# Optimization experiments

Measured on AMD Instinct MI355X. Metric: run time of the kernel, lower is better.

Reference implementation:

```python
import jax, jax.numpy as jnp
import numpy as np

D = 2048; Nl = 2; Nh = 32; Nkv = 8; V = 32000; Dh = 5632; Lm = 4096
B = 1; L = 2048; E = 1e-5
DHEAD = D // Nh  # 64


def setup_inputs() -> dict:
    key = jax.random.key(0)
    ks = jax.random.split(key, 10)
    s = 0.02
    rn = lambda k, shape: jax.random.normal(k, shape, jnp.float32) * s
    emb = rn(ks[0], (V, D))
    wq = rn(ks[1], (Nl, D, D))
    wk = rn(ks[2], (Nl, D, D * Nkv // Nh))
    wv = rn(ks[3], (Nl, D, D * Nkv // Nh))
    wa = rn(ks[4], (Nl, D, D))
    wg = rn(ks[5], (Nl, D, Dh))
    wu = rn(ks[6], (Nl, D, Dh))
    wd = rn(ks[7], (Nl, Dh, D))
    w_an = jnp.ones((Nl, D), jnp.float32)
    w_fn = jnp.ones((Nl, D), jnp.float32)
    w_on = jnp.ones((D,), jnp.float32)
    w_out = rn(ks[8], (D, V))
    # RoPE tables (interleaved-pair convention, matching reshape(..., -1, 2))
    theta = 1.0 / (10000.0 ** (jnp.arange(0, DHEAD, 2, dtype=jnp.float32) / DHEAD))
    freqs = jnp.outer(jnp.arange(Lm, dtype=jnp.float32), theta)  # [Lm, DHEAD//2]
    cos = jnp.cos(freqs)
    sin = jnp.sin(freqs)
    ti = jax.random.randint(ks[9], (B, L), 0, V)
    return dict(ti=ti, emb=emb, wq=wq, wk=wk, wv=wv, wa=wa, w_an=w_an, w_fn=w_fn,
                wg=wg, wu=wu, wd=wd, w_on=w_on, w_out=w_out, cos=cos, sin=sin)


def _rmsnorm(x, w):
    return x * jax.lax.rsqrt(jnp.mean(x * x, -1, keepdims=True) + E) * w


def _rope(x, cos, sin):
    # x: [B, L, H, DHEAD]; cos/sin: [1, L, 1, DHEAD//2]; interleaved pairs
    xs = x.reshape(*x.shape[:-1], DHEAD // 2, 2)
    xr, xi = xs[..., 0], xs[..., 1]
    r1 = xr * cos - xi * sin
    i1 = xr * sin + xi * cos
    return jnp.stack([r1, i1], axis=-1).reshape(x.shape)


def reference(ti, emb, wq, wk, wv, wa, w_an, w_fn, wg, wu, wd, w_on, w_out, cos, sin):
    cos_l = cos[:L].reshape(1, L, 1, DHEAD // 2)
    sin_l = sin[:L].reshape(1, L, 1, DHEAD // 2)
    mask = jnp.triu(jnp.full((1, 1, L, L), -jnp.inf, jnp.float32), 1)
    scale = 1.0 / jnp.sqrt(jnp.float32(DHEAD))
    rep = Nh // Nkv
    x = emb[ti]  # [B, L, D]
    for l in range(Nl):
        h = _rmsnorm(x, w_an[l])
        q = (h @ wq[l]).reshape(B, L, Nh, DHEAD)
        k = (h @ wk[l]).reshape(B, L, Nkv, DHEAD)
        v = (h @ wv[l]).reshape(B, L, Nkv, DHEAD)
        q = _rope(q, cos_l, sin_l)
        k = _rope(k, cos_l, sin_l)
        kx = jnp.repeat(k, rep, axis=2)  # GQA expand -> [B, L, Nh, DHEAD]
        vx = jnp.repeat(v, rep, axis=2)
        a = jnp.einsum('blhd,bmhd->bhlm', q, kx) * scale
        p = jax.nn.softmax(a + mask, axis=-1)
        sa = jnp.einsum('bhlm,bmhd->blhd', p, vx).reshape(B, L, D)
        x = x + sa @ wa[l]
        hf = _rmsnorm(x, w_fn[l])
        x = x + (jax.nn.silu(hf @ wg[l]) * (hf @ wu[l])) @ wd[l]
    return _rmsnorm(x, w_on) @ w_out  # [B, L, V]
```

## Files before the change

kernel.cpp:

```cpp
#include <hip/hip_runtime.h>
#include <hip/hip_bf16.h>

#define DMODEL 2048
#define LSEQ   2048
#define NHEAD  32
#define NKVH   8
#define DHEAD  64
#define DFF    5632
#define VOCAB  32000

typedef __attribute__((ext_vector_type(8))) short bf16x8;
typedef __attribute__((ext_vector_type(4))) float f32x4;
typedef __attribute__((ext_vector_type(8))) unsigned short ushort8;

__device__ __forceinline__ void gload_lds16(const __hip_bfloat16* g, __hip_bfloat16* l) {
  __builtin_amdgcn_global_load_lds((const void __attribute__((address_space(1)))*)g,
                                   (void __attribute__((address_space(3)))*)l, 16, 0, 0);
}

__device__ __forceinline__ float bfbits2f(unsigned short u) {
  return __uint_as_float(((unsigned int)u) << 16);
}
__device__ __forceinline__ unsigned short f2bfbits(float f) {
  unsigned int x = __float_as_uint(f);
  return (unsigned short)((x + 0x7fffu + ((x >> 16) & 1u)) >> 16);
}

__global__ __launch_bounds__(256) void embed_k(const int* __restrict__ ti,
                                               const float* __restrict__ emb,
                                               float* __restrict__ x) {
  const int row = blockIdx.x;
  const int t = threadIdx.x;
  const int tok = ti[row];
  const float4* s = (const float4*)(emb + (size_t)tok * DMODEL);
  float4* d = (float4*)(x + (size_t)row * DMODEL);
  d[t] = s[t];
  d[t + 256] = s[t + 256];
}

__global__ __launch_bounds__(256) void rmsnorm_k(const float* __restrict__ x,
                                                 const float* __restrict__ w,
                                                 __hip_bfloat16* __restrict__ out) {
  const int row = blockIdx.x;
  const int t = threadIdx.x;
  const float4* xr = (const float4*)(x + (size_t)row * DMODEL);
  float4 a = xr[t];
  float4 b = xr[t + 256];
  float ss = a.x*a.x + a.y*a.y + a.z*a.z + a.w*a.w
           + b.x*b.x + b.y*b.y + b.z*b.z + b.w*b.w;
  #pragma unroll
  for (int m = 32; m >= 1; m >>= 1) ss += __shfl_xor(ss, m);
  __shared__ float red[4];
  if ((t & 63) == 0) red[t >> 6] = ss;
  __syncthreads();
  const float tot = red[0] + red[1] + red[2] + red[3];
  const float sc = rsqrtf(tot * (1.0f / DMODEL) + 1e-5f);
  const float4* w4 = (const float4*)w;
  float4 wa_ = w4[t], wb_ = w4[t + 256];
  __hip_bfloat16* o = out + (size_t)row * DMODEL;
  o[4*t + 0] = __float2bfloat16(a.x * sc * wa_.x);
  o[4*t + 1] = __float2bfloat16(a.y * sc * wa_.y);
  o[4*t + 2] = __float2bfloat16(a.z * sc * wa_.z);
  o[4*t + 3] = __float2bfloat16(a.w * sc * wa_.w);
  o[1024 + 4*t + 0] = __float2bfloat16(b.x * sc * wb_.x);
  o[1024 + 4*t + 1] = __float2bfloat16(b.y * sc * wb_.y);
  o[1024 + 4*t + 2] = __float2bfloat16(b.z * sc * wb_.z);
  o[1024 + 4*t + 3] = __float2bfloat16(b.w * sc * wb_.w);
}

__global__ __launch_bounds__(256) void transpose_k(const float* __restrict__ src,
                                                   __hip_bfloat16* __restrict__ dst,
                                                   int K, int N) {
  __shared__ float tile[64 * 65];
  const int kb = blockIdx.x * 64;
  const int nb = blockIdx.y * 64;
  const int t = threadIdx.x;
  #pragma unroll
  for (int i = 0; i < 16; ++i) {
    const int idx = t + 256 * i;
    const int r = idx >> 6, c = idx & 63;
    tile[r * 65 + c] = src[(size_t)(kb + r) * N + nb + c];
  }
  __syncthreads();
  #pragma unroll
  for (int i = 0; i < 16; ++i) {
    const int idx = t + 256 * i;
    const int n = idx >> 6, k = idx & 63;
    dst[(size_t)(nb + n) * K + kb + k] = __float2bfloat16(tile[k * 65 + n]);
  }
}

template <int EPI>
__global__ __launch_bounds__(256) void gemm_bt(const __hip_bfloat16* __restrict__ A,
                                               const __hip_bfloat16* __restrict__ Bt,
                                               float* __restrict__ Cf,
                                               __hip_bfloat16* __restrict__ Cb,
                                               int M, int N, int K) {
  __shared__ __align__(16) __hip_bfloat16 As[128 * 32];
  __shared__ __align__(16) __hip_bfloat16 Bs[128 * 32];
  const int tid = threadIdx.x;
  const int wave = tid >> 6;
  const int lane = tid & 63;
  const int nbx = M >> 7;
  const int nwg = nbx * (N >> 7);
  const int orig = blockIdx.y * nbx + blockIdx.x;
  const int wid = (orig & 7) * (nwg >> 3) + (orig >> 3);
  const int tm = (wid % nbx) << 7;
  const int tn = (wid / nbx) << 7;
  const int wr = (wave >> 1) * 64;
  const int wc = (wave & 1) * 64;
  const int fr = lane & 15;
  const int fg = lane >> 4;
  const f32x4 fzero = {0.f, 0.f, 0.f, 0.f};
  f32x4 acc[4][4];
  #pragma unroll
  for (int i = 0; i < 4; ++i)
    #pragma unroll
    for (int j = 0; j < 4; ++j) acc[i][j] = fzero;
  const int srow = wave * 32 + (lane >> 2);
  const int scol = (lane & 3) * 8;
  const __hip_bfloat16* gA = A + (size_t)(tm + srow) * K + scol;
  const __hip_bfloat16* gB = Bt + (size_t)(tn + srow) * K + scol;
  __hip_bfloat16* lA = &As[wave * 1024];
  __hip_bfloat16* lB = &Bs[wave * 1024];
  for (int k0 = 0; k0 < K; k0 += 32) {
    gload_lds16(gA, lA);
    gload_lds16(gA + (size_t)16 * K, lA + 512);
    gload_lds16(gB, lB);
    gload_lds16(gB + (size_t)16 * K, lB + 512);
    gA += 32; gB += 32;
    __syncthreads();
    bf16x8 af[4], bfr[4];
    #pragma unroll
    for (int i = 0; i < 4; ++i) af[i] = *(const bf16x8*)&As[(wr + i * 16 + fr) * 32 + fg * 8];
    #pragma unroll
    for (int j = 0; j < 4; ++j) bfr[j] = *(const bf16x8*)&Bs[(wc + j * 16 + fr) * 32 + fg * 8];
    #pragma unroll
    for (int i = 0; i < 4; ++i)
      #pragma unroll
      for (int j = 0; j < 4; ++j)
        acc[i][j] = __builtin_amdgcn_mfma_f32_16x16x32_bf16(af[i], bfr[j], acc[i][j], 0, 0, 0);
    __syncthreads();
  }
  #pragma unroll
  for (int i = 0; i < 4; ++i)
    #pragma unroll
    for (int j = 0; j < 4; ++j)
      #pragma unroll
      for (int r = 0; r < 4; ++r) {
        const int row = tm + wr + i * 16 + fg * 4 + r;
        const int col = tn + wc + j * 16 + fr;
        const float v = acc[i][j][r];
        if (EPI == 0) Cf[(size_t)row * N + col] = v;
        else if (EPI == 1) Cb[(size_t)row * N + col] = __float2bfloat16(v);
        else Cf[(size_t)row * N + col] += v;
      }
}

template <int EPI>
__global__ __launch_bounds__(512, 2) void gemm8p(const __hip_bfloat16* __restrict__ A,
                                                 const __hip_bfloat16* __restrict__ Bt,
                                                 float* __restrict__ Cf,
                                                 __hip_bfloat16* __restrict__ Cb,
                                                 int M, int N, int K) {
  __shared__ __align__(16) __hip_bfloat16 lds[2][2][256 * 64];
  const int tid = threadIdx.x;
  const int wave = tid >> 6;
  const int lane = tid & 63;
  const int nbx = M >> 8;
  const int nwg = nbx * (N >> 8);
  const int orig = blockIdx.y * nbx + blockIdx.x;
  const int wid = (orig & 7) * (nwg >> 3) + (orig >> 3);
  const int tm = (wid % nbx) << 8;
  const int tn = (wid / nbx) << 8;
  const int wm = wave >> 2;
  const int wn = wave & 3;
  const int fr = lane & 15;
  const int fg = lane >> 4;
  const int l3 = lane >> 3;
  const int l7 = lane & 7;
  const int swzcol = (l3 ^ l7) << 3;
  const size_t sK = (size_t)K;

  const __hip_bfloat16* pA = A + (size_t)(tm + wave * 8 + l3) * sK + swzcol;
  const __hip_bfloat16* pB = Bt + (size_t)(tn + wave * 8 + l3) * sK + swzcol;

  #pragma unroll
  for (int j = 0; j < 4; ++j) {
    gload_lds16(pA + (size_t)(j * 64) * sK, &lds[0][0][(j * 64 + wave * 8) * 64]);
    gload_lds16(pB + (size_t)(j * 64) * sK, &lds[0][1][(j * 64 + wave * 8) * 64]);
  }
  pA += 64; pB += 64;
  #pragma unroll
  for (int j = 0; j < 4; ++j) {
    gload_lds16(pA + (size_t)(j * 64) * sK, &lds[1][0][(j * 64 + wave * 8) * 64]);
    gload_lds16(pB + (size_t)(j * 64) * sK, &lds[1][1][(j * 64 + wave * 8) * 64]);
  }
  pA += 64; pB += 64;

  const f32x4 fzero = {0.f, 0.f, 0.f, 0.f};
  f32x4 acc[8][4];
  #pragma unroll
  for (int i = 0; i < 8; ++i)
    #pragma unroll
    for (int j = 0; j < 4; ++j) acc[i][j] = fzero;

  const int wmo = wm * 128;
  const int wno = wn * 64;
  const int rswz = (fr & 7) << 4;
  const int ct0 = ((fg * 16) ^ rswz) >> 1;
  const int ct1 = ((64 + fg * 16) ^ rswz) >> 1;

  asm volatile("s_waitcnt vmcnt(8)" ::: "memory");
  __builtin_amdgcn_s_barrier();
  __builtin_amdgcn_sched_barrier(0);

  const int NT = K >> 6;
  for (int kt = 0; kt < NT; ++kt) {
    const int cur = kt & 1;
    const __hip_bfloat16* LA = &lds[cur][0][0];
    const __hip_bfloat16* LB = &lds[cur][1][0];
    bf16x8 av[8][2], bv[4][2];
    #pragma unroll
    for (int mi = 0; mi < 8; ++mi) {
      av[mi][0] = *(const bf16x8*)&LA[(wmo + mi * 16 + fr) * 64 + ct0];
      av[mi][1] = *(const bf16x8*)&LA[(wmo + mi * 16 + fr) * 64 + ct1];
    }
    #pragma unroll
    for (int ni = 0; ni < 4; ++ni) {
      bv[ni][0] = *(const bf16x8*)&LB[(wno + ni * 16 + fr) * 64 + ct0];
      bv[ni][1] = *(const bf16x8*)&LB[(wno + ni * 16 + fr) * 64 + ct1];
    }
    asm volatile("s_waitcnt lgkmcnt(0)" ::: "memory");
    __builtin_amdgcn_sched_barrier(0);
    __builtin_amdgcn_s_barrier();
    __builtin_amdgcn_sched_barrier(0);
    const bool pre = (kt + 2 < NT);
    #pragma unroll
    for (int q = 0; q < 4; ++q) {
      if (pre) {
        gload_lds16(pA + (size_t)(q * 64) * sK, &lds[cur][0][(q * 64 + wave * 8) * 64]);
        gload_lds16(pB + (size_t)(q * 64) * sK, &lds[cur][1][(q * 64 + wave * 8) * 64]);
      }
      const int mb = (q & 1) * 4;
      const int nb = (q >> 1) * 2;
      __builtin_amdgcn_s_setprio(1);
      #pragma unroll
      for (int mi = 0; mi < 4; ++mi)
        #pragma unroll
        for (int ni = 0; ni < 2; ++ni) {
          acc[mb + mi][nb + ni] = __builtin_amdgcn_mfma_f32_16x16x32_bf16(
              av[mb + mi][0], bv[nb + ni][0], acc[mb + mi][nb + ni], 0, 0, 0);
          acc[mb + mi][nb + ni] = __builtin_amdgcn_mfma_f32_16x16x32_bf16(
              av[mb + mi][1], bv[nb + ni][1], acc[mb + mi][nb + ni], 0, 0, 0);
        }
      __builtin_amdgcn_s_setprio(0);
    }
    if (pre) { pA += 64; pB += 64; }
    if (kt + 1 < NT) {
      if (pre) asm volatile("s_waitcnt vmcnt(8)" ::: "memory");
      else     asm volatile("s_waitcnt vmcnt(0)" ::: "memory");
      __builtin_amdgcn_s_barrier();
      __builtin_amdgcn_sched_barrier(0);
    }
  }
  #pragma unroll
  for (int mf = 0; mf < 8; ++mf)
    #pragma unroll
    for (int nf = 0; nf < 4; ++nf)
      #pragma unroll
      for (int r = 0; r < 4; ++r) {
        const int row = tm + wmo + mf * 16 + fg * 4 + r;
        const int col = tn + wno + nf * 16 + fr;
        const float v = acc[mf][nf][r];
        if (EPI == 0) Cf[(size_t)row * N + col] = v;
        else if (EPI == 1) Cb[(size_t)row * N + col] = __float2bfloat16(v);
        else Cf[(size_t)row * N + col] += v;
      }
}

__global__ __launch_bounds__(256) void rope_k(__hip_bfloat16* __restrict__ qkv,
                                              const float* __restrict__ cosT,
                                              const float* __restrict__ sinT) {
  const int row = blockIdx.x;
  const int t = threadIdx.x;
  unsigned int* base = (unsigned int*)(qkv + (size_t)row * 3072);
  #pragma unroll
  for (int p = t; p < 1280; p += 256) {
    const int hp = p >> 5;
    const int i = p & 31;
    const unsigned int packed = base[hp * 32 + i];
    const float x0 = bfbits2f((unsigned short)(packed & 0xffffu));
    const float x1 = bfbits2f((unsigned short)(packed >> 16));
    const float c = cosT[row * 32 + i];
    const float s = sinT[row * 32 + i];
    const float r0 = x0 * c - x1 * s;
    const float r1 = x0 * s + x1 * c;
    base[hp * 32 + i] = (unsigned int)f2bfbits(r0) | ((unsigned int)f2bfbits(r1) << 16);
  }
}

__global__ __launch_bounds__(256) void attn_k(const __hip_bfloat16* __restrict__ qkv,
                                              __hip_bfloat16* __restrict__ out) {
  const int h = blockIdx.x;
  const int qt = blockIdx.y;
  const int tid = threadIdx.x;
  const int wave = tid >> 6;
  const int lane = tid & 63;
  const int fr = lane & 15;
  const int fg = lane >> 4;
  const int qb = qt * 64;
  const int kcol = DMODEL + (h >> 2) * DHEAD;
  const int vcol = DMODEL + NKVH * DHEAD + (h >> 2) * DHEAD;
  __shared__ __align__(16) __hip_bfloat16 Ks[64 * 72];
  __shared__ __align__(16) __hip_bfloat16 Vt[64 * 72];
  __shared__ __align__(16) __hip_bfloat16 Ps[4][16 * 72];
  bf16x8 qf[2];
  {
    const __hip_bfloat16* qp = qkv + (size_t)(qb + wave * 16 + fr) * 3072 + h * DHEAD + fg * 8;
    qf[0] = *(const bf16x8*)qp;
    qf[1] = *(const bf16x8*)(qp + 32);
  }
  const f32x4 fzero = {0.f, 0.f, 0.f, 0.f};
  float m_run[4], l_run[4];
  f32x4 o[4];
  #pragma unroll
  for (int r = 0; r < 4; ++r) { m_run[r] = -1e30f; l_run[r] = 0.f; }
  #pragma unroll
  for (int c = 0; c < 4; ++c) o[c] = fzero;

  const int sr = tid >> 2;
  const int sc = (tid & 3) * 16;
  for (int t = 0; t <= qt; ++t) {
    const __hip_bfloat16* kp = qkv + (size_t)(t * 64 + sr) * 3072 + kcol + sc;
    *(float4*)&Ks[sr * 72 + sc] = *(const float4*)kp;
    *(float4*)&Ks[sr * 72 + sc + 8] = *(const float4*)(kp + 8);
    const __hip_bfloat16* vp = qkv + (size_t)(t * 64 + sr) * 3072 + vcol + sc;
    ushort8 v0 = *(const ushort8*)vp;
    ushort8 v1 = *(const ushort8*)(vp + 8);
    unsigned short* vt = (unsigned short*)Vt;
    #pragma unroll
    for (int i = 0; i < 8; ++i) {
      vt[(sc + i) * 72 + sr] = v0[i];
      vt[(sc + 8 + i) * 72 + sr] = v1[i];
    }
    __syncthreads();
    f32x4 s[4];
    #pragma unroll
    for (int c = 0; c < 4; ++c) {
      s[c] = fzero;
      #pragma unroll
      for (int ks = 0; ks < 2; ++ks) {
        bf16x8 kf = *(const bf16x8*)&Ks[(c * 16 + fr) * 72 + ks * 32 + fg * 8];
        s[c] = __builtin_amdgcn_mfma_f32_16x16x32_bf16(qf[ks], kf, s[c], 0, 0, 0);
      }
    }
    const int rowg = qb + wave * 16 + fg * 4;
    #pragma unroll
    for (int c = 0; c < 4; ++c)
      #pragma unroll
      for (int r = 0; r < 4; ++r) {
        float v = s[c][r] * 0.125f;
        if (t * 64 + c * 16 + fr > rowg + r) v = -1e30f;
        s[c][r] = v;
      }
    #pragma unroll
    for (int r = 0; r < 4; ++r) {
      float pm = fmaxf(fmaxf(s[0][r], s[1][r]), fmaxf(s[2][r], s[3][r]));
      pm = fmaxf(pm, __shfl_xor(pm, 1));
      pm = fmaxf(pm, __shfl_xor(pm, 2));
      pm = fmaxf(pm, __shfl_xor(pm, 4));
      pm = fmaxf(pm, __shfl_xor(pm, 8));
      const float mn = fmaxf(m_run[r], pm);
      const float al = __expf(m_run[r] - mn);
      m_run[r] = mn;
      float rs = 0.f;
      #pragma unroll
      for (int c = 0; c < 4; ++c) { float p = __expf(s[c][r] - mn); s[c][r] = p; rs += p; }
      rs += __shfl_xor(rs, 1);
      rs += __shfl_xor(rs, 2);
      rs += __shfl_xor(rs, 4);
      rs += __shfl_xor(rs, 8);
      l_run[r] = l_run[r] * al + rs;
      #pragma unroll
      for (int c = 0; c < 4; ++c) o[c][r] *= al;
    }
    unsigned short* pw = (unsigned short*)Ps[wave];
    #pragma unroll
    for (int c = 0; c < 4; ++c)
      #pragma unroll
      for (int r = 0; r < 4; ++r)
        pw[(fg * 4 + r) * 72 + c * 16 + fr] = f2bfbits(s[c][r]);
    #pragma unroll
    for (int ks = 0; ks < 2; ++ks) {
      bf16x8 pf = *(const bf16x8*)&Ps[wave][fr * 72 + ks * 32 + fg * 8];
      #pragma unroll
      for (int c = 0; c < 4; ++c) {
        bf16x8 vf = *(const bf16x8*)&Vt[(c * 16 + fr) * 72 + ks * 32 + fg * 8];
        o[c] = __builtin_amdgcn_mfma_f32_16x16x32_bf16(pf, vf, o[c], 0, 0, 0);
      }
    }
    __syncthreads();
  }
  #pragma unroll
  for (int c = 0; c < 4; ++c)
    #pragma unroll
    for (int r = 0; r < 4; ++r)
      out[(size_t)(qb + wave * 16 + fg * 4 + r) * DMODEL + h * DHEAD + c * 16 + fr] =
          __float2bfloat16(o[c][r] / l_run[r]);
}

__global__ __launch_bounds__(256) void silu_k(const __hip_bfloat16* __restrict__ gu,
                                              __hip_bfloat16* __restrict__ mb) {
  const int row = blockIdx.x;
  const int t = threadIdx.x;
  const ushort8* g8 = (const ushort8*)(gu + (size_t)row * (2 * DFF));
  const ushort8* u8 = (const ushort8*)(gu + (size_t)row * (2 * DFF) + DFF);
  ushort8* m8 = (ushort8*)(mb + (size_t)row * DFF);
  for (int j = t; j * 8 < DFF; j += 256) {
    ushort8 g = g8[j], u = u8[j];
    ushort8 ov;
    #pragma unroll
    for (int i = 0; i < 8; ++i) {
      const float gf = bfbits2f(g[i]);
      const float uf = bfbits2f(u[i]);
      ov[i] = f2bfbits(gf / (1.f + __expf(-gf)) * uf);
    }
    m8[j] = ov;
  }
}

extern "C" void kernel_launch(void* const* d_in, const int* in_sizes, int n_in,
                              void* d_out, int out_size, void* d_ws, size_t ws_size,
                              hipStream_t stream) {
  const int* ti = (const int*)d_in[0];
  const float* emb = (const float*)d_in[1];
  const float* wq = (const float*)d_in[2];
  const float* wk = (const float*)d_in[3];
  const float* wv = (const float*)d_in[4];
  const float* wa = (const float*)d_in[5];
  const float* w_an = (const float*)d_in[6];
  const float* w_fn = (const float*)d_in[7];
  const float* wg = (const float*)d_in[8];
  const float* wu = (const float*)d_in[9];
  const float* wd = (const float*)d_in[10];
  const float* w_on = (const float*)d_in[11];
  const float* w_out = (const float*)d_in[12];
  const float* cosT = (const float*)d_in[13];
  const float* sinT = (const float*)d_in[14];
  float* outp = (float*)d_out;

  char* ws = (char*)d_ws;
  float* x            = (float*)(ws + 0);
  __hip_bfloat16* h   = (__hip_bfloat16*)(ws + 16777216);
  __hip_bfloat16* qkv = (__hip_bfloat16*)(ws + 25165824);
  __hip_bfloat16* att = (__hip_bfloat16*)(ws + 37748736);
  __hip_bfloat16* gu  = (__hip_bfloat16*)(ws + 46137344);
  __hip_bfloat16* mb  = (__hip_bfloat16*)(ws + 92274688);
  __hip_bfloat16* wTqkv = (__hip_bfloat16*)(ws + 115343360);
  __hip_bfloat16* wTa   = (__hip_bfloat16*)(ws + 127926272);
  __hip_bfloat16* wTgu  = (__hip_bfloat16*)(ws + 136314880);
  __hip_bfloat16* wTd   = (__hip_bfloat16*)(ws + 182452224);
  __hip_bfloat16* wTout = (__hip_bfloat16*)(ws + 25165824);
  (void)in_sizes; (void)n_in; (void)out_size; (void)ws_size;

  const dim3 blk(256);
  embed_k<<<2048, blk, 0, stream>>>(ti, emb, x);
  for (int l = 0; l < 2; ++l) {
    transpose_k<<<dim3(32, 32), blk, 0, stream>>>(wq + (size_t)l * 2048 * 2048, wTqkv, 2048, 2048);
    transpose_k<<<dim3(32, 8),  blk, 0, stream>>>(wk + (size_t)l * 2048 * 512, wTqkv + (size_t)2048 * 2048, 2048, 512);
    transpose_k<<<dim3(32, 8),  blk, 0, stream>>>(wv + (size_t)l * 2048 * 512, wTqkv + (size_t)2560 * 2048, 2048, 512);
    transpose_k<<<dim3(32, 32), blk, 0, stream>>>(wa + (size_t)l * 2048 * 2048, wTa, 2048, 2048);
    transpose_k<<<dim3(32, 88), blk, 0, stream>>>(wg + (size_t)l * 2048 * 5632, wTgu, 2048, 5632);
    transpose_k<<<dim3(32, 88), blk, 0, stream>>>(wu + (size_t)l * 2048 * 5632, wTgu + (size_t)5632 * 2048, 2048, 5632);
    transpose_k<<<dim3(88, 32), blk, 0, stream>>>(wd + (size_t)l * 5632 * 2048, wTd, 5632, 2048);

    rmsnorm_k<<<2048, blk, 0, stream>>>(x, w_an + l * 2048, h);
    gemm_bt<1><<<dim3(16, 24), blk, 0, stream>>>(h, wTqkv, nullptr, qkv, 2048, 3072, 2048);
    rope_k<<<2048, blk, 0, stream>>>(qkv, cosT, sinT);
    attn_k<<<dim3(32, 32), blk, 0, stream>>>(qkv, att);
    gemm_bt<2><<<dim3(16, 16), blk, 0, stream>>>(att, wTa, x, nullptr, 2048, 2048, 2048);

    rmsnorm_k<<<2048, blk, 0, stream>>>(x, w_fn + l * 2048, h);
    gemm8p<1><<<dim3(8, 44), dim3(512), 0, stream>>>(h, wTgu, nullptr, gu, 2048, 11264, 2048);
    silu_k<<<2048, blk, 0, stream>>>(gu, mb);
    gemm_bt<2><<<dim3(16, 16), blk, 0, stream>>>(mb, wTd, x, nullptr, 2048, 2048, 5632);
  }
  transpose_k<<<dim3(32, 500), blk, 0, stream>>>(w_out, wTout, 2048, 32000);
  rmsnorm_k<<<2048, blk, 0, stream>>>(x, w_on, h);
  gemm8p<0><<<dim3(8, 125), dim3(512), 0, stream>>>(h, wTout, outp, nullptr, 2048, 32000, 2048);
}
```

Baseline: 1.469 ms.

## Transpose QK MFMA so each lane owns one query row; pack V transpose stores

The QK^T MFMA operands are swapped so the score tile comes out transposed. Each lane then holds 16 keys of a single query row, so the softmax running max and sum become one scalar per lane and need only two cross-lane shuffles instead of four per row. The V transpose into LDS now packs two rows into 32-bit stores, and P is written to LDS as packed 64-bit stores, cutting the number of LDS write instructions. The cost is extra shuffles to hand the rescale factors and final normalizers back to the output layout, which adds some complexity to the attention inner loop.

Result: faster. 1.427 ms (-2.8%).

```diff
diff --git a/kernel.cpp b/kernel.cpp
--- a/kernel.cpp
+++ b/kernel.cpp
@@ -322,27 +322,31 @@
     qf[1] = *(const bf16x8*)(qp + 32);
   }
   const f32x4 fzero = {0.f, 0.f, 0.f, 0.f};
-  float m_run[4], l_run[4];
+  float m_run = -1e30f, l_run = 0.f;
   f32x4 o[4];
-  #pragma unroll
-  for (int r = 0; r < 4; ++r) { m_run[r] = -1e30f; l_run[r] = 0.f; }
   #pragma unroll
   for (int c = 0; c < 4; ++c) o[c] = fzero;
 
   const int sr = tid >> 2;
   const int sc = (tid & 3) * 16;
+  const int vpr = tid >> 3;
+  const int vg = tid & 7;
+  const int myq = qb + wave * 16 + fr;
+
   for (int t = 0; t <= qt; ++t) {
     const __hip_bfloat16* kp = qkv + (size_t)(t * 64 + sr) * 3072 + kcol + sc;
     *(float4*)&Ks[sr * 72 + sc] = *(const float4*)kp;
     *(float4*)&Ks[sr * 72 + sc + 8] = *(const float4*)(kp + 8);
-    const __hip_bfloat16* vp = qkv + (size_t)(t * 64 + sr) * 3072 + vcol + sc;
-    ushort8 v0 = *(const ushort8*)vp;
-    ushort8 v1 = *(const ushort8*)(vp + 8);
-    unsigned short* vt = (unsigned short*)Vt;
-    #pragma unroll
-    for (int i = 0; i < 8; ++i) {
-      vt[(sc + i) * 72 + sr] = v0[i];
-      vt[(sc + 8 + i) * 72 + sr] = v1[i];
+    {
+      const __hip_bfloat16* vp0 = qkv + (size_t)(t * 64 + 2 * vpr) * 3072 + vcol + vg * 8;
+      ushort8 va = *(const ushort8*)vp0;
+      ushort8 vb = *(const ushort8*)(vp0 + 3072);
+      unsigned short* vt = (unsigned short*)Vt;
+      #pragma unroll
+      for (int i = 0; i < 8; ++i) {
+        unsigned int pk = (unsigned int)va[i] | ((unsigned int)vb[i] << 16);
+        *(unsigned int*)(vt + (vg * 8 + i) * 72 + 2 * vpr) = pk;
+      }
     }
     __syncthreads();
     f32x4 s[4];
@@ -352,45 +356,53 @@
       #pragma unroll
       for (int ks = 0; ks < 2; ++ks) {
         bf16x8 kf = *(const bf16x8*)&Ks[(c * 16 + fr) * 72 + ks * 32 + fg * 8];
-        s[c] = __builtin_amdgcn_mfma_f32_16x16x32_bf16(qf[ks], kf, s[c], 0, 0, 0);
-      }
-    }
-    const int rowg = qb + wave * 16 + fg * 4;
+        s[c] = __builtin_amdgcn_mfma_f32_16x16x32_bf16(kf, qf[ks], s[c], 0, 0, 0);
+      }
+    }
+    float pm = -1e30f;
     #pragma unroll
     for (int c = 0; c < 4; ++c)
       #pragma unroll
       for (int r = 0; r < 4; ++r) {
         float v = s[c][r] * 0.125f;
-        if (t * 64 + c * 16 + fr > rowg + r) v = -1e30f;
+        if (t * 64 + c * 16 + fg * 4 + r > myq) v = -1e30f;
         s[c][r] = v;
-      }
-    #pragma unroll
-    for (int r = 0; r < 4; ++r) {
-      float pm = fmaxf(fmaxf(s[0][r], s[1][r]), fmaxf(s[2][r], s[3][r]));
-      pm = fmaxf(pm, __shfl_xor(pm, 1));
-      pm = fmaxf(pm, __shfl_xor(pm, 2));
-      pm = fmaxf(pm, __shfl_xor(pm, 4));
-      pm = fmaxf(pm, __shfl_xor(pm, 8));
-      const float mn = fmaxf(m_run[r], pm);
-      const float al = __expf(m_run[r] - mn);
-      m_run[r] = mn;
-      float rs = 0.f;
-      #pragma unroll
-      for (int c = 0; c < 4; ++c) { float p = __expf(s[c][r] - mn); s[c][r] = p; rs += p; }
-      rs += __shfl_xor(rs, 1);
-      rs += __shfl_xor(rs, 2);
-      rs += __shfl_xor(rs, 4);
-      rs += __shfl_xor(rs, 8);
-      l_run[r] = l_run[r] * al + rs;
-      #pragma unroll
-      for (int c = 0; c < 4; ++c) o[c][r] *= al;
-    }
-    unsigned short* pw = (unsigned short*)Ps[wave];
+        pm = fmaxf(pm, v);
+      }
+    pm = fmaxf(pm, __shfl_xor(pm, 16));
+    pm = fmaxf(pm, __shfl_xor(pm, 32));
+    const float mn = fmaxf(m_run, pm);
+    const float al = __expf(m_run - mn);
+    m_run = mn;
+    float rs = 0.f;
     #pragma unroll
     for (int c = 0; c < 4; ++c)
       #pragma unroll
-      for (int r = 0; r < 4; ++r)
-        pw[(fg * 4 + r) * 72 + c * 16 + fr] = f2bfbits(s[c][r]);
+      for (int r = 0; r < 4; ++r) {
+        float p = __expf(s[c][r] - mn);
+        s[c][r] = p;
+        rs += p;
+      }
+    rs += __shfl_xor(rs, 16);
+    rs += __shfl_xor(rs, 32);
+    l_run = l_run * al + rs;
+    float als[4];
+    #pragma unroll
+    for (int r = 0; r < 4; ++r) als[r] = __shfl(al, fg * 4 + r);
+    #pragma unroll
+    for (int c = 0; c < 4; ++c)
+      #pragma unroll
+      for (int r = 0; r < 4; ++r) o[c][r] *= als[r];
+    {
+      unsigned short* pw = (unsigned short*)Ps[wave];
+      #pragma unroll
+      for (int c = 0; c < 4; ++c) {
+        unsigned int lo = (unsigned int)f2bfbits(s[c][0]) | ((unsigned int)f2bfbits(s[c][1]) << 16);
+        unsigned int hi = (unsigned int)f2bfbits(s[c][2]) | ((unsigned int)f2bfbits(s[c][3]) << 16);
+        uint2 pk; pk.x = lo; pk.y = hi;
+        *(uint2*)(pw + fr * 72 + c * 16 + fg * 4) = pk;
+      }
+    }
     #pragma unroll
     for (int ks = 0; ks < 2; ++ks) {
       bf16x8 pf = *(const bf16x8*)&Ps[wave][fr * 72 + ks * 32 + fg * 8];
@@ -402,12 +414,15 @@
     }
     __syncthreads();
   }
+  float lq[4];
+  #pragma unroll
+  for (int r = 0; r < 4; ++r) lq[r] = __shfl(l_run, fg * 4 + r);
   #pragma unroll
   for (int c = 0; c < 4; ++c)
     #pragma unroll
     for (int r = 0; r < 4; ++r)
       out[(size_t)(qb + wave * 16 + fg * 4 + r) * DMODEL + h * DHEAD + c * 16 + fr] =
-          __float2bfloat16(o[c][r] / l_run[r]);
+          __float2bfloat16(o[c][r] / lq[r]);
 }
 
 __global__ __launch_bounds__(256) void silu_k(const __hip_bfloat16* __restrict__ gu,
```
